# Optimization experiments

Measured on AMD Instinct MI355X. Metric: run time of the kernel, lower is better.

The kernel has to match this reference:

```python
import jax, jax.numpy as jnp
import numpy as np

NUM_USERS = 100000
NUM_ITEMS = 50000
DIM = 64
N_LAYERS = 3
L_W = 1e-4
E0 = 600000          # raw user-item interactions
B = 8192             # BPR batch size
N_NODES = NUM_USERS + NUM_ITEMS


def setup_inputs() -> dict:
    key = jax.random.key(0)
    k1, k2, k3, k4, k5, k6, k7 = jax.random.split(key, 7)
    return {
        "Gu": jax.random.normal(k1, (NUM_USERS, DIM), jnp.float32) * 0.1,
        "Gi": jax.random.normal(k2, (NUM_ITEMS, DIM), jnp.float32) * 0.1,
        "edge_user": jax.random.randint(k3, (E0,), 0, NUM_USERS),
        "edge_item": jax.random.randint(k4, (E0,), 0, NUM_ITEMS),
        "user": jax.random.randint(k5, (B,), 0, NUM_USERS),
        "pos": jax.random.randint(k6, (B,), 0, NUM_ITEMS),
        "neg": jax.random.randint(k7, (B,), 0, NUM_ITEMS),
    }


def _propagate(Gu, Gi, src, dst):
    # symmetric normalized adjacency (gcn_norm, no self-loops, as in LGConv)
    deg = jax.ops.segment_sum(jnp.ones_like(src, jnp.float32), dst,
                              num_segments=N_NODES)
    dinv = jnp.where(deg > 0, jax.lax.rsqrt(deg), 0.0)
    w = dinv[src] * dinv[dst]                      # [E]
    x = jnp.concatenate([Gu, Gi], axis=0)          # [N, D]
    acc = x
    h = x
    for _ in range(N_LAYERS):
        # SpMM: h' = D^-1/2 A D^-1/2 h  (gather + weighted scatter-add)
        h = jax.ops.segment_sum(w[:, None] * h[src], dst,
                                num_segments=N_NODES)
        acc = acc + h
    emb = acc / (N_LAYERS + 1)                     # mean over all layers
    return emb[:NUM_USERS], emb[NUM_USERS:]


def reference(Gu, Gi, edge_user, edge_item, user, pos, neg):
    # symmetrize bipartite edges; items offset by NUM_USERS
    src = jnp.concatenate([edge_user, edge_item + NUM_USERS])
    dst = jnp.concatenate([edge_item + NUM_USERS, edge_user])
    gu, gi = _propagate(Gu, Gi, src, dst)
    gu_u, gi_p, gi_n = gu[user], gi[pos], gi[neg]  # [B, D]
    xu_pos = jnp.sum(gu_u * gi_p, axis=1)
    xu_neg = jnp.sum(gu_u * gi_n, axis=1)
    mf_loss = -jnp.mean(jax.nn.log_sigmoid(xu_pos - xu_neg))
    reg = L_W * 0.5 * (jnp.sum(gu_u ** 2) + jnp.sum(gi_p ** 2)
                       + jnp.sum(gi_n ** 2)) / B
    return mf_loss + reg
```

## Files before the change

kernel.cpp:

```cpp
#include <hip/hip_runtime.h>

#define NUSERS 100000
#define NITEMS 50000
#define NNODES 150000
#define DIM 64
#define E0 600000
#define E2 (2 * E0)
#define BB 8192
#define LW 1e-4f
#define NN16 150016
#define LOSS_BLOCKS 128
#define UBLK 6250
#define IBLK 3125

#define NBUCK 1172
#define CHUNK_E 2048
#define CHUNKS 293
#define CPAD 320
#define BCAP 3072

__device__ __forceinline__ float bf_lo(unsigned u) { return __uint_as_float(u << 16); }
__device__ __forceinline__ float bf_hi(unsigned u) { return __uint_as_float(u & 0xffff0000u); }
__device__ __forceinline__ unsigned rne16(float x) {
  unsigned u = __float_as_uint(x);
  return (u + 0x7fffu + ((u >> 16) & 1u)) >> 16;
}
__device__ __forceinline__ unsigned pack2(float lo, float hi) {
  return rne16(lo) | (rne16(hi) << 16);
}

__global__ __launch_bounds__(256) void k_bcount(const int* __restrict__ eu,
                                                const int* __restrict__ ei,
                                                int* __restrict__ cnt) {
  __shared__ int h[NBUCK];
  for (int i = threadIdx.x; i < NBUCK; i += 256) h[i] = 0;
  __syncthreads();
  int c = blockIdx.x;
  int e0 = c * CHUNK_E;
  int e1 = min(e0 + CHUNK_E, E0);
  for (int e = e0 + threadIdx.x; e < e1; e += 256) {
    int u = eu[e];
    int it = NUSERS + ei[e];
    atomicAdd(&h[u >> 7], 1);
    atomicAdd(&h[it >> 7], 1);
  }
  __syncthreads();
  for (int i = threadIdx.x; i < NBUCK; i += 256) cnt[(size_t)i * CPAD + c] = h[i];
}

__global__ __launch_bounds__(256) void k_bscan1(int* __restrict__ cnt,
                                                int* __restrict__ btot) {
  int b = blockIdx.x * 4 + (threadIdx.x >> 6);
  int lane = threadIdx.x & 63;
  int* row = cnt + (size_t)b * CPAD;
  int carry = 0;
  for (int c0 = 0; c0 < CHUNKS; c0 += 64) {
    int c = c0 + lane;
    int v = (c < CHUNKS) ? row[c] : 0;
    int s = v;
    #pragma unroll
    for (int m = 1; m < 64; m <<= 1) {
      int t = __shfl_up(s, m);
      if (lane >= m) s += t;
    }
    if (c < CHUNKS) row[c] = carry + s - v;
    carry += __shfl(s, 63);
  }
  if (lane == 63) btot[b] = carry;
}

__global__ void k_bbase(const int* __restrict__ btot, int* __restrict__ bbase) {
  __shared__ int s[1024];
  int t = threadIdx.x;
  int i0 = 2 * t, i1 = 2 * t + 1;
  int v0 = (i0 < NBUCK) ? btot[i0] : 0;
  int v1 = (i1 < NBUCK) ? btot[i1] : 0;
  s[t] = v0 + v1;
  __syncthreads();
  for (int off = 1; off < 1024; off <<= 1) {
    int x = 0;
    if (t >= off) x = s[t - off];
    __syncthreads();
    if (t >= off) s[t] += x;
    __syncthreads();
  }
  int base = (t > 0) ? s[t - 1] : 0;
  if (i0 < NBUCK) bbase[i0] = base;
  if (i1 < NBUCK) bbase[i1] = base + v0;
}

__global__ __launch_bounds__(256) void k_bscatter(const int* __restrict__ eu,
                                                  const int* __restrict__ ei,
                                                  const int* __restrict__ cnt,
                                                  const int* __restrict__ bbase,
                                                  unsigned* __restrict__ pk) {
  __shared__ int soff[NBUCK];
  int c = blockIdx.x;
  for (int i = threadIdx.x; i < NBUCK; i += 256)
    soff[i] = cnt[(size_t)i * CPAD + c] + bbase[i];
  __syncthreads();
  int e0 = c * CHUNK_E;
  int e1 = min(e0 + CHUNK_E, E0);
  for (int e = e0 + threadIdx.x; e < e1; e += 256) {
    int u = eu[e];
    int it = NUSERS + ei[e];
    int s1 = atomicAdd(&soff[u >> 7], 1);
    pk[s1] = ((unsigned)it << 7) | (unsigned)(u & 127);
    int s2 = atomicAdd(&soff[it >> 7], 1);
    pk[s2] = ((unsigned)u << 7) | (unsigned)(it & 127);
  }
}

__global__ __launch_bounds__(256) void k_bucket_csr(
    const unsigned* __restrict__ pk, const int* __restrict__ btot,
    const int* __restrict__ bbase, int* __restrict__ deg, int* __restrict__ ptr,
    float* __restrict__ dinv, int* __restrict__ col,
    const float4* __restrict__ Gu4, const float4* __restrict__ Gi4,
    uint2* __restrict__ h0) {
  __shared__ unsigned sitm[BCAP];
  __shared__ int ldeg[128], lscan[128], lcnt[128];
  __shared__ float sdv[128];
  int b = blockIdx.x;
  int base = bbase[b];
  int n = btot[b];
  for (int i = threadIdx.x; i < n; i += 256)
    if (i < BCAP) sitm[i] = pk[base + i];
  if (threadIdx.x < 128) { ldeg[threadIdx.x] = 0; lcnt[threadIdx.x] = 0; }
  __syncthreads();
  for (int i = threadIdx.x; i < n; i += 256) {
    unsigned p = (i < BCAP) ? sitm[i] : pk[base + i];
    atomicAdd(&ldeg[p & 127], 1);
  }
  __syncthreads();
  if (threadIdx.x < 128) lscan[threadIdx.x] = ldeg[threadIdx.x];
  __syncthreads();
  for (int off = 1; off < 128; off <<= 1) {
    int t = 0;
    if (threadIdx.x < 128 && (int)threadIdx.x >= off) t = lscan[threadIdx.x - off];
    __syncthreads();
    if (threadIdx.x < 128 && (int)threadIdx.x >= off) lscan[threadIdx.x] += t;
    __syncthreads();
  }
  int node = b * 128 + threadIdx.x;
  if (threadIdx.x < 128) {
    int d = ldeg[threadIdx.x];
    lscan[threadIdx.x] -= d;
    float dv = d > 0 ? rsqrtf((float)d) : 0.0f;
    sdv[threadIdx.x] = dv;
    if (node < NNODES) {
      deg[node] = d;
      ptr[node] = base + lscan[threadIdx.x];
      dinv[node] = dv;
    }
  }
  __syncthreads();
  for (int i = threadIdx.x; i < n; i += 256) {
    unsigned p = (i < BCAP) ? sitm[i] : pk[base + i];
    int dl = p & 127;
    int pos = base + lscan[dl] + atomicAdd(&lcnt[dl], 1);
    col[pos] = (int)(p >> 7);
  }
  for (int w = threadIdx.x; w < 128 * 16; w += 256) {
    int nl = w >> 4, q = w & 15;
    int nd = b * 128 + nl;
    if (nd < NNODES) {
      float dv = sdv[nl];
      float4 v = (nd < NUSERS) ? Gu4[(size_t)nd * 16 + q]
                               : Gi4[(size_t)(nd - NUSERS) * 16 + q];
      h0[(size_t)nd * 16 + q] =
          make_uint2(pack2(dv * v.x, dv * v.y), pack2(dv * v.z, dv * v.w));
    }
  }
}

__global__ __launch_bounds__(512) void k_spmm2(
    const int* __restrict__ ptr, const int* __restrict__ deg,
    const int* __restrict__ col, const float* __restrict__ dinv,
    const uint4* __restrict__ h, uint4* __restrict__ hout) {
  int wid = threadIdx.x >> 6;
  int lane = threadIdx.x & 63;
  int sub = lane >> 3;
  int q = lane & 7;
  int gA, coff;
  const uint4* hsrc;
  if (blockIdx.x < UBLK) {
    gA = blockIdx.x * 16 + wid * 2;
    coff = NUSERS;
    hsrc = h + (size_t)NUSERS * 8;
  } else {
    gA = NUSERS + (blockIdx.x - UBLK) * 16 + wid * 2;
    coff = 0;
    hsrc = h;
  }
  int gB = gA + 1;
  int stA = ptr[gA], dgA = deg[gA];
  int stB = ptr[gB], dgB = deg[gB];
  float dnA = dinv[gA], dnB = dinv[gB];
  int cA = (sub < dgA) ? col[stA + sub] : -1;
  int cB = (sub < dgB) ? col[stB + sub] : -1;
  uint4 xA = {0, 0, 0, 0}, xB = {0, 0, 0, 0};
  if (cA >= 0) xA = hsrc[(size_t)(cA - coff) * 8 + q];
  if (cB >= 0) xB = hsrc[(size_t)(cB - coff) * 8 + q];
  float aA0 = bf_lo(xA.x), aA1 = bf_hi(xA.x), aA2 = bf_lo(xA.y), aA3 = bf_hi(xA.y);
  float aA4 = bf_lo(xA.z), aA5 = bf_hi(xA.z), aA6 = bf_lo(xA.w), aA7 = bf_hi(xA.w);
  float aB0 = bf_lo(xB.x), aB1 = bf_hi(xB.x), aB2 = bf_lo(xB.y), aB3 = bf_hi(xB.y);
  float aB4 = bf_lo(xB.z), aB5 = bf_hi(xB.z), aB6 = bf_lo(xB.w), aB7 = bf_hi(xB.w);
  for (int j = stA + 8 + sub; j < stA + dgA; j += 8) {
    int c = col[j];
    uint4 x = hsrc[(size_t)(c - coff) * 8 + q];
    aA0 += bf_lo(x.x); aA1 += bf_hi(x.x); aA2 += bf_lo(x.y); aA3 += bf_hi(x.y);
    aA4 += bf_lo(x.z); aA5 += bf_hi(x.z); aA6 += bf_lo(x.w); aA7 += bf_hi(x.w);
  }
  for (int j = stB + 8 + sub; j < stB + dgB; j += 8) {
    int c = col[j];
    uint4 x = hsrc[(size_t)(c - coff) * 8 + q];
    aB0 += bf_lo(x.x); aB1 += bf_hi(x.x); aB2 += bf_lo(x.y); aB3 += bf_hi(x.y);
    aB4 += bf_lo(x.z); aB5 += bf_hi(x.z); aB6 += bf_lo(x.w); aB7 += bf_hi(x.w);
  }
  #pragma unroll
  for (int m = 8; m <= 32; m <<= 1) {
    aA0 += __shfl_xor(aA0, m); aA1 += __shfl_xor(aA1, m);
    aA2 += __shfl_xor(aA2, m); aA3 += __shfl_xor(aA3, m);
    aA4 += __shfl_xor(aA4, m); aA5 += __shfl_xor(aA5, m);
    aA6 += __shfl_xor(aA6, m); aA7 += __shfl_xor(aA7, m);
    aB0 += __shfl_xor(aB0, m); aB1 += __shfl_xor(aB1, m);
    aB2 += __shfl_xor(aB2, m); aB3 += __shfl_xor(aB3, m);
    aB4 += __shfl_xor(aB4, m); aB5 += __shfl_xor(aB5, m);
    aB6 += __shfl_xor(aB6, m); aB7 += __shfl_xor(aB7, m);
  }
  if (sub == 0) {
    float sA = dnA * dnA;
    float sB = dnB * dnB;
    hout[(size_t)gA * 8 + q] = make_uint4(pack2(aA0 * sA, aA1 * sA), pack2(aA2 * sA, aA3 * sA),
                                          pack2(aA4 * sA, aA5 * sA), pack2(aA6 * sA, aA7 * sA));
    hout[(size_t)gB * 8 + q] = make_uint4(pack2(aB0 * sB, aB1 * sB), pack2(aB2 * sB, aB3 * sB),
                                          pack2(aB4 * sB, aB5 * sB), pack2(aB6 * sB, aB7 * sB));
  }
}

__device__ __forceinline__ int decode_node(int k, const int* __restrict__ usr,
                                           const int* __restrict__ pos,
                                           const int* __restrict__ neg, int* coff) {
  if (k < BB) { *coff = NUSERS; return usr[k]; }
  if (k < 2 * BB) { *coff = 0; return NUSERS + pos[k - BB]; }
  *coff = 0; return NUSERS + neg[k - 2 * BB];
}

__global__ __launch_bounds__(512) void k_spmm_batch(
    const int* __restrict__ usr, const int* __restrict__ pos, const int* __restrict__ neg,
    const int* __restrict__ ptr, const int* __restrict__ deg,
    const int* __restrict__ col, const float* __restrict__ dinv,
    const uint4* __restrict__ h, uint4* __restrict__ hout) {
  int wid = threadIdx.x >> 6;
  int lane = threadIdx.x & 63;
  int sub = lane >> 3;
  int q = lane & 7;
  int k0 = blockIdx.x * 16 + wid * 2;
  int cofA, cofB;
  int gA = decode_node(k0, usr, pos, neg, &cofA);
  int gB = decode_node(k0 + 1, usr, pos, neg, &cofB);
  const uint4* hsA = h + (size_t)cofA * 8;
  const uint4* hsB = h + (size_t)cofB * 8;
  int stA = ptr[gA], dgA = deg[gA];
  int stB = ptr[gB], dgB = deg[gB];
  float dnA = dinv[gA], dnB = dinv[gB];
  int cA = (sub < dgA) ? col[stA + sub] : -1;
  int cB = (sub < dgB) ? col[stB + sub] : -1;
  uint4 xA = {0, 0, 0, 0}, xB = {0, 0, 0, 0};
  if (cA >= 0) xA = hsA[(size_t)(cA - cofA) * 8 + q];
  if (cB >= 0) xB = hsB[(size_t)(cB - cofB) * 8 + q];
  float aA0 = bf_lo(xA.x), aA1 = bf_hi(xA.x), aA2 = bf_lo(xA.y), aA3 = bf_hi(xA.y);
  float aA4 = bf_lo(xA.z), aA5 = bf_hi(xA.z), aA6 = bf_lo(xA.w), aA7 = bf_hi(xA.w);
  float aB0 = bf_lo(xB.x), aB1 = bf_hi(xB.x), aB2 = bf_lo(xB.y), aB3 = bf_hi(xB.y);
  float aB4 = bf_lo(xB.z), aB5 = bf_hi(xB.z), aB6 = bf_lo(xB.w), aB7 = bf_hi(xB.w);
  for (int j = stA + 8 + sub; j < stA + dgA; j += 8) {
    int c = col[j];
    uint4 x = hsA[(size_t)(c - cofA) * 8 + q];
    aA0 += bf_lo(x.x); aA1 += bf_hi(x.x); aA2 += bf_lo(x.y); aA3 += bf_hi(x.y);
    aA4 += bf_lo(x.z); aA5 += bf_hi(x.z); aA6 += bf_lo(x.w); aA7 += bf_hi(x.w);
  }
  for (int j = stB + 8 + sub; j < stB + dgB; j += 8) {
    int c = col[j];
    uint4 x = hsB[(size_t)(c - cofB) * 8 + q];
    aB0 += bf_lo(x.x); aB1 += bf_hi(x.x); aB2 += bf_lo(x.y); aB3 += bf_hi(x.y);
    aB4 += bf_lo(x.z); aB5 += bf_hi(x.z); aB6 += bf_lo(x.w); aB7 += bf_hi(x.w);
  }
  #pragma unroll
  for (int m = 8; m <= 32; m <<= 1) {
    aA0 += __shfl_xor(aA0, m); aA1 += __shfl_xor(aA1, m);
    aA2 += __shfl_xor(aA2, m); aA3 += __shfl_xor(aA3, m);
    aA4 += __shfl_xor(aA4, m); aA5 += __shfl_xor(aA5, m);
    aA6 += __shfl_xor(aA6, m); aA7 += __shfl_xor(aA7, m);
    aB0 += __shfl_xor(aB0, m); aB1 += __shfl_xor(aB1, m);
    aB2 += __shfl_xor(aB2, m); aB3 += __shfl_xor(aB3, m);
    aB4 += __shfl_xor(aB4, m); aB5 += __shfl_xor(aB5, m);
    aB6 += __shfl_xor(aB6, m); aB7 += __shfl_xor(aB7, m);
  }
  if (sub == 0) {
    float sA = dnA * dnA;
    float sB = dnB * dnB;
    hout[(size_t)gA * 8 + q] = make_uint4(pack2(aA0 * sA, aA1 * sA), pack2(aA2 * sA, aA3 * sA),
                                          pack2(aA4 * sA, aA5 * sA), pack2(aA6 * sA, aA7 * sA));
    hout[(size_t)gB * 8 + q] = make_uint4(pack2(aB0 * sB, aB1 * sB), pack2(aB2 * sB, aB3 * sB),
                                          pack2(aB4 * sB, aB5 * sB), pack2(aB6 * sB, aB7 * sB));
  }
}

__global__ void k_loss(const int* __restrict__ usr, const int* __restrict__ pos,
                       const int* __restrict__ neg, const int* __restrict__ deg,
                       const float4* __restrict__ Gu4, const float4* __restrict__ Gi4,
                       const uint2* __restrict__ h1, const uint2* __restrict__ h2,
                       const uint2* __restrict__ h3, float* __restrict__ bpart) {
  __shared__ float sL[4], sR[4];
  int wid = threadIdx.x >> 6;
  int lane = threadIdx.x & 63;
  int r = lane >> 4;
  int q = lane & 15;
  int gw = blockIdx.x * 4 + wid;
  int nw = gridDim.x * 4;
  const float s = 0.25f;
  float accL = 0.0f, accR = 0.0f;
  for (int b4 = gw; b4 < BB / 4; b4 += nw) {
    int b = b4 * 4 + r;
    int iu = usr[b], ip = pos[b], ig = neg[b];
    float sdu = sqrtf((float)deg[iu]);
    float sdp = sqrtf((float)deg[NUSERS + ip]);
    float sdn = sqrtf((float)deg[NUSERS + ig]);
    size_t ou = (size_t)iu * 16 + q;
    size_t op = ((size_t)NUSERS + ip) * 16 + q;
    size_t on = ((size_t)NUSERS + ig) * 16 + q;
    float4 u = Gu4[ou];
    float4 p = Gi4[(size_t)ip * 16 + q];
    float4 g = Gi4[(size_t)ig * 16 + q];
    float4 su = {0, 0, 0, 0}, sp = {0, 0, 0, 0}, sg = {0, 0, 0, 0};
    uint2 v;
    v = h1[ou]; su.x += bf_lo(v.x); su.y += bf_hi(v.x); su.z += bf_lo(v.y); su.w += bf_hi(v.y);
    v = h2[ou]; su.x += bf_lo(v.x); su.y += bf_hi(v.x); su.z += bf_lo(v.y); su.w += bf_hi(v.y);
    v = h3[ou]; su.x += bf_lo(v.x); su.y += bf_hi(v.x); su.z += bf_lo(v.y); su.w += bf_hi(v.y);
    v = h1[op]; sp.x += bf_lo(v.x); sp.y += bf_hi(v.x); sp.z += bf_lo(v.y); sp.w += bf_hi(v.y);
    v = h2[op]; sp.x += bf_lo(v.x); sp.y += bf_hi(v.x); sp.z += bf_lo(v.y); sp.w += bf_hi(v.y);
    v = h3[op]; sp.x += bf_lo(v.x); sp.y += bf_hi(v.x); sp.z += bf_lo(v.y); sp.w += bf_hi(v.y);
    v = h1[on]; sg.x += bf_lo(v.x); sg.y += bf_hi(v.x); sg.z += bf_lo(v.y); sg.w += bf_hi(v.y);
    v = h2[on]; sg.x += bf_lo(v.x); sg.y += bf_hi(v.x); sg.z += bf_lo(v.y); sg.w += bf_hi(v.y);
    v = h3[on]; sg.x += bf_lo(v.x); sg.y += bf_hi(v.x); sg.z += bf_lo(v.y); sg.w += bf_hi(v.y);
    u.x = (u.x + sdu * su.x) * s; u.y = (u.y + sdu * su.y) * s;
    u.z = (u.z + sdu * su.z) * s; u.w = (u.w + sdu * su.w) * s;
    p.x = (p.x + sdp * sp.x) * s; p.y = (p.y + sdp * sp.y) * s;
    p.z = (p.z + sdp * sp.z) * s; p.w = (p.w + sdp * sp.w) * s;
    g.x = (g.x + sdn * sg.x) * s; g.y = (g.y + sdn * sg.y) * s;
    g.z = (g.z + sdn * sg.z) * s; g.w = (g.w + sdn * sg.w) * s;
    float dp = u.x * p.x + u.y * p.y + u.z * p.z + u.w * p.w;
    float dn = u.x * g.x + u.y * g.y + u.z * g.z + u.w * g.w;
    float rg = u.x * u.x + u.y * u.y + u.z * u.z + u.w * u.w
             + p.x * p.x + p.y * p.y + p.z * p.z + p.w * p.w
             + g.x * g.x + g.y * g.y + g.z * g.z + g.w * g.w;
    #pragma unroll
    for (int m = 1; m <= 8; m <<= 1) {
      dp += __shfl_xor(dp, m);
      dn += __shfl_xor(dn, m);
      rg += __shfl_xor(rg, m);
    }
    if (q == 0) {
      float diff = dp - dn;
      accL -= fminf(diff, 0.0f) - log1pf(expf(-fabsf(diff)));
      accR += rg;
    }
  }
  accL += __shfl_xor(accL, 16); accR += __shfl_xor(accR, 16);
  accL += __shfl_xor(accL, 32); accR += __shfl_xor(accR, 32);
  if (lane == 0) { sL[wid] = accL; sR[wid] = accR; }
  __syncthreads();
  if (threadIdx.x == 0) {
    bpart[blockIdx.x] = sL[0] + sL[1] + sL[2] + sL[3];
    bpart[LOSS_BLOCKS + blockIdx.x] = sR[0] + sR[1] + sR[2] + sR[3];
  }
}

__global__ void k_final(const float* __restrict__ bpart, float* __restrict__ out) {
  int lane = threadIdx.x;
  float l = bpart[lane] + bpart[lane + 64];
  float r = bpart[LOSS_BLOCKS + lane] + bpart[LOSS_BLOCKS + lane + 64];
  for (int off = 32; off > 0; off >>= 1) {
    l += __shfl_down(l, off);
    r += __shfl_down(r, off);
  }
  if (lane == 0) out[0] = l * (1.0f / BB) + LW * 0.5f * r * (1.0f / BB);
}

extern "C" void kernel_launch(void* const* d_in, const int* in_sizes, int n_in,
                              void* d_out, int out_size, void* d_ws, size_t ws_size,
                              hipStream_t stream) {
  const float* Gu = (const float*)d_in[0];
  const float* Gi = (const float*)d_in[1];
  const int* eu  = (const int*)d_in[2];
  const int* ei  = (const int*)d_in[3];
  const int* usr = (const int*)d_in[4];
  const int* pos = (const int*)d_in[5];
  const int* neg = (const int*)d_in[6];
  float* out = (float*)d_out;

  int* deg    = (int*)d_ws;
  int* ptr    = deg + NN16;
  float* dinv = (float*)(ptr + NN16);
  int* col    = (int*)(dinv + NN16);
  uint2* h0   = (uint2*)(col + E2);
  uint2* h1   = h0 + (size_t)NNODES * 16;
  uint2* h2   = h1 + (size_t)NNODES * 16;
  uint2* h3   = h2 + (size_t)NNODES * 16;
  float* bpart = (float*)(h3 + (size_t)NNODES * 16);

  unsigned* pk = (unsigned*)h1;
  int* cnt     = (int*)h2;
  int* btot    = (int*)h3;
  int* bbase   = btot + 1280;

  const float4* Gu4 = (const float4*)Gu;
  const float4* Gi4 = (const float4*)Gi;

  k_bcount<<<CHUNKS, 256, 0, stream>>>(eu, ei, cnt);
  k_bscan1<<<NBUCK / 4, 256, 0, stream>>>(cnt, btot);
  k_bbase<<<1, 1024, 0, stream>>>(btot, bbase);
  k_bscatter<<<CHUNKS, 256, 0, stream>>>(eu, ei, cnt, bbase, pk);
  k_bucket_csr<<<NBUCK, 256, 0, stream>>>(pk, btot, bbase, deg, ptr, dinv, col,
                                          Gu4, Gi4, h0);

  k_spmm2<<<UBLK + IBLK, 512, 0, stream>>>(ptr, deg, col, dinv,
                                           (const uint4*)h0, (uint4*)h1);
  k_spmm2<<<UBLK + IBLK, 512, 0, stream>>>(ptr, deg, col, dinv,
                                           (const uint4*)h1, (uint4*)h2);
  k_spmm_batch<<<(3 * BB) / 16, 512, 0, stream>>>(usr, pos, neg, ptr, deg, col, dinv,
                                                  (const uint4*)h2, (uint4*)h3);

  k_loss<<<LOSS_BLOCKS, 256, 0, stream>>>(usr, pos, neg, deg, Gu4, Gi4, h1, h2, h3, bpart);
  k_final<<<1, 64, 0, stream>>>(bpart, out);
}
```

Measured before the change: 242.7 us.

## Map one 8-lane group per node in SpMM instead of splitting edges across lanes

Both SpMM kernels stop giving each wave two nodes with edges split across eight sub-groups and a shuffle reduction. Each 8-thread group now owns one node and walks its whole neighbour list serially, two edges per iteration. This removes the shuffle reduction and the idle lanes on low-degree nodes, at the cost of per-lane load imbalance when degrees vary. The loss kernel also moves from 128 to 512 blocks, and the final reduction loops over the larger partial array.

```diff
diff --git a/kernel.cpp b/kernel.cpp
--- a/kernel.cpp
+++ b/kernel.cpp
@@ -9,9 +9,9 @@
 #define BB 8192
 #define LW 1e-4f
 #define NN16 150016
-#define LOSS_BLOCKS 128
-#define UBLK 6250
-#define IBLK 3125
+#define LOSS_BLOCKS 512
+#define SPMM_B 2344
+#define SPMMB_B 384
 
 #define NBUCK 1172
 #define CHUNK_E 2048
@@ -177,65 +177,38 @@
     const int* __restrict__ ptr, const int* __restrict__ deg,
     const int* __restrict__ col, const float* __restrict__ dinv,
     const uint4* __restrict__ h, uint4* __restrict__ hout) {
-  int wid = threadIdx.x >> 6;
-  int lane = threadIdx.x & 63;
-  int sub = lane >> 3;
-  int q = lane & 7;
-  int gA, coff;
+  int t = blockIdx.x * 512 + threadIdx.x;
+  int g = t >> 3;
+  int q = t & 7;
+  if (g >= NNODES) return;
+  int coff;
   const uint4* hsrc;
-  if (blockIdx.x < UBLK) {
-    gA = blockIdx.x * 16 + wid * 2;
-    coff = NUSERS;
-    hsrc = h + (size_t)NUSERS * 8;
-  } else {
-    gA = NUSERS + (blockIdx.x - UBLK) * 16 + wid * 2;
-    coff = 0;
-    hsrc = h;
-  }
-  int gB = gA + 1;
-  int stA = ptr[gA], dgA = deg[gA];
-  int stB = ptr[gB], dgB = deg[gB];
-  float dnA = dinv[gA], dnB = dinv[gB];
-  int cA = (sub < dgA) ? col[stA + sub] : -1;
-  int cB = (sub < dgB) ? col[stB + sub] : -1;
-  uint4 xA = {0, 0, 0, 0}, xB = {0, 0, 0, 0};
-  if (cA >= 0) xA = hsrc[(size_t)(cA - coff) * 8 + q];
-  if (cB >= 0) xB = hsrc[(size_t)(cB - coff) * 8 + q];
-  float aA0 = bf_lo(xA.x), aA1 = bf_hi(xA.x), aA2 = bf_lo(xA.y), aA3 = bf_hi(xA.y);
-  float aA4 = bf_lo(xA.z), aA5 = bf_hi(xA.z), aA6 = bf_lo(xA.w), aA7 = bf_hi(xA.w);
-  float aB0 = bf_lo(xB.x), aB1 = bf_hi(xB.x), aB2 = bf_lo(xB.y), aB3 = bf_hi(xB.y);
-  float aB4 = bf_lo(xB.z), aB5 = bf_hi(xB.z), aB6 = bf_lo(xB.w), aB7 = bf_hi(xB.w);
-  for (int j = stA + 8 + sub; j < stA + dgA; j += 8) {
-    int c = col[j];
-    uint4 x = hsrc[(size_t)(c - coff) * 8 + q];
-    aA0 += bf_lo(x.x); aA1 += bf_hi(x.x); aA2 += bf_lo(x.y); aA3 += bf_hi(x.y);
-    aA4 += bf_lo(x.z); aA5 += bf_hi(x.z); aA6 += bf_lo(x.w); aA7 += bf_hi(x.w);
-  }
-  for (int j = stB + 8 + sub; j < stB + dgB; j += 8) {
-    int c = col[j];
-    uint4 x = hsrc[(size_t)(c - coff) * 8 + q];
-    aB0 += bf_lo(x.x); aB1 += bf_hi(x.x); aB2 += bf_lo(x.y); aB3 += bf_hi(x.y);
-    aB4 += bf_lo(x.z); aB5 += bf_hi(x.z); aB6 += bf_lo(x.w); aB7 += bf_hi(x.w);
-  }
-  #pragma unroll
-  for (int m = 8; m <= 32; m <<= 1) {
-    aA0 += __shfl_xor(aA0, m); aA1 += __shfl_xor(aA1, m);
-    aA2 += __shfl_xor(aA2, m); aA3 += __shfl_xor(aA3, m);
-    aA4 += __shfl_xor(aA4, m); aA5 += __shfl_xor(aA5, m);
-    aA6 += __shfl_xor(aA6, m); aA7 += __shfl_xor(aA7, m);
-    aB0 += __shfl_xor(aB0, m); aB1 += __shfl_xor(aB1, m);
-    aB2 += __shfl_xor(aB2, m); aB3 += __shfl_xor(aB3, m);
-    aB4 += __shfl_xor(aB4, m); aB5 += __shfl_xor(aB5, m);
-    aB6 += __shfl_xor(aB6, m); aB7 += __shfl_xor(aB7, m);
-  }
-  if (sub == 0) {
-    float sA = dnA * dnA;
-    float sB = dnB * dnB;
-    hout[(size_t)gA * 8 + q] = make_uint4(pack2(aA0 * sA, aA1 * sA), pack2(aA2 * sA, aA3 * sA),
-                                          pack2(aA4 * sA, aA5 * sA), pack2(aA6 * sA, aA7 * sA));
-    hout[(size_t)gB * 8 + q] = make_uint4(pack2(aB0 * sB, aB1 * sB), pack2(aB2 * sB, aB3 * sB),
-                                          pack2(aB4 * sB, aB5 * sB), pack2(aB6 * sB, aB7 * sB));
-  }
+  if (g < NUSERS) { coff = NUSERS; hsrc = h + (size_t)NUSERS * 8; }
+  else { coff = 0; hsrc = h; }
+  int st = ptr[g], dg = deg[g];
+  float dn = dinv[g];
+  float a0 = 0, a1 = 0, a2 = 0, a3 = 0, a4 = 0, a5 = 0, a6 = 0, a7 = 0;
+  int jend = st + dg;
+  int j = st;
+  for (; j + 2 <= jend; j += 2) {
+    int c0 = col[j] - coff;
+    int c1 = col[j + 1] - coff;
+    uint4 x0 = hsrc[(size_t)c0 * 8 + q];
+    uint4 x1 = hsrc[(size_t)c1 * 8 + q];
+    a0 += bf_lo(x0.x); a1 += bf_hi(x0.x); a2 += bf_lo(x0.y); a3 += bf_hi(x0.y);
+    a4 += bf_lo(x0.z); a5 += bf_hi(x0.z); a6 += bf_lo(x0.w); a7 += bf_hi(x0.w);
+    a0 += bf_lo(x1.x); a1 += bf_hi(x1.x); a2 += bf_lo(x1.y); a3 += bf_hi(x1.y);
+    a4 += bf_lo(x1.z); a5 += bf_hi(x1.z); a6 += bf_lo(x1.w); a7 += bf_hi(x1.w);
+  }
+  if (j < jend) {
+    int c0 = col[j] - coff;
+    uint4 x0 = hsrc[(size_t)c0 * 8 + q];
+    a0 += bf_lo(x0.x); a1 += bf_hi(x0.x); a2 += bf_lo(x0.y); a3 += bf_hi(x0.y);
+    a4 += bf_lo(x0.z); a5 += bf_hi(x0.z); a6 += bf_lo(x0.w); a7 += bf_hi(x0.w);
+  }
+  float s = dn * dn;
+  hout[(size_t)g * 8 + q] = make_uint4(pack2(a0 * s, a1 * s), pack2(a2 * s, a3 * s),
+                                       pack2(a4 * s, a5 * s), pack2(a6 * s, a7 * s));
 }
 
 __device__ __forceinline__ int decode_node(int k, const int* __restrict__ usr,
@@ -251,59 +224,36 @@
     const int* __restrict__ ptr, const int* __restrict__ deg,
     const int* __restrict__ col, const float* __restrict__ dinv,
     const uint4* __restrict__ h, uint4* __restrict__ hout) {
-  int wid = threadIdx.x >> 6;
-  int lane = threadIdx.x & 63;
-  int sub = lane >> 3;
-  int q = lane & 7;
-  int k0 = blockIdx.x * 16 + wid * 2;
-  int cofA, cofB;
-  int gA = decode_node(k0, usr, pos, neg, &cofA);
-  int gB = decode_node(k0 + 1, usr, pos, neg, &cofB);
-  const uint4* hsA = h + (size_t)cofA * 8;
-  const uint4* hsB = h + (size_t)cofB * 8;
-  int stA = ptr[gA], dgA = deg[gA];
-  int stB = ptr[gB], dgB = deg[gB];
-  float dnA = dinv[gA], dnB = dinv[gB];
-  int cA = (sub < dgA) ? col[stA + sub] : -1;
-  int cB = (sub < dgB) ? col[stB + sub] : -1;
-  uint4 xA = {0, 0, 0, 0}, xB = {0, 0, 0, 0};
-  if (cA >= 0) xA = hsA[(size_t)(cA - cofA) * 8 + q];
-  if (cB >= 0) xB = hsB[(size_t)(cB - cofB) * 8 + q];
-  float aA0 = bf_lo(xA.x), aA1 = bf_hi(xA.x), aA2 = bf_lo(xA.y), aA3 = bf_hi(xA.y);
-  float aA4 = bf_lo(xA.z), aA5 = bf_hi(xA.z), aA6 = bf_lo(xA.w), aA7 = bf_hi(xA.w);
-  float aB0 = bf_lo(xB.x), aB1 = bf_hi(xB.x), aB2 = bf_lo(xB.y), aB3 = bf_hi(xB.y);
-  float aB4 = bf_lo(xB.z), aB5 = bf_hi(xB.z), aB6 = bf_lo(xB.w), aB7 = bf_hi(xB.w);
-  for (int j = stA + 8 + sub; j < stA + dgA; j += 8) {
-    int c = col[j];
-    uint4 x = hsA[(size_t)(c - cofA) * 8 + q];
-    aA0 += bf_lo(x.x); aA1 += bf_hi(x.x); aA2 += bf_lo(x.y); aA3 += bf_hi(x.y);
-    aA4 += bf_lo(x.z); aA5 += bf_hi(x.z); aA6 += bf_lo(x.w); aA7 += bf_hi(x.w);
-  }
-  for (int j = stB + 8 + sub; j < stB + dgB; j += 8) {
-    int c = col[j];
-    uint4 x = hsB[(size_t)(c - cofB) * 8 + q];
-    aB0 += bf_lo(x.x); aB1 += bf_hi(x.x); aB2 += bf_lo(x.y); aB3 += bf_hi(x.y);
-    aB4 += bf_lo(x.z); aB5 += bf_hi(x.z); aB6 += bf_lo(x.w); aB7 += bf_hi(x.w);
-  }
-  #pragma unroll
-  for (int m = 8; m <= 32; m <<= 1) {
-    aA0 += __shfl_xor(aA0, m); aA1 += __shfl_xor(aA1, m);
-    aA2 += __shfl_xor(aA2, m); aA3 += __shfl_xor(aA3, m);
-    aA4 += __shfl_xor(aA4, m); aA5 += __shfl_xor(aA5, m);
-    aA6 += __shfl_xor(aA6, m); aA7 += __shfl_xor(aA7, m);
-    aB0 += __shfl_xor(aB0, m); aB1 += __shfl_xor(aB1, m);
-    aB2 += __shfl_xor(aB2, m); aB3 += __shfl_xor(aB3, m);
-    aB4 += __shfl_xor(aB4, m); aB5 += __shfl_xor(aB5, m);
-    aB6 += __shfl_xor(aB6, m); aB7 += __shfl_xor(aB7, m);
-  }
-  if (sub == 0) {
-    float sA = dnA * dnA;
-    float sB = dnB * dnB;
-    hout[(size_t)gA * 8 + q] = make_uint4(pack2(aA0 * sA, aA1 * sA), pack2(aA2 * sA, aA3 * sA),
-                                          pack2(aA4 * sA, aA5 * sA), pack2(aA6 * sA, aA7 * sA));
-    hout[(size_t)gB * 8 + q] = make_uint4(pack2(aB0 * sB, aB1 * sB), pack2(aB2 * sB, aB3 * sB),
-                                          pack2(aB4 * sB, aB5 * sB), pack2(aB6 * sB, aB7 * sB));
-  }
+  int t = blockIdx.x * 512 + threadIdx.x;
+  int k = t >> 3;
+  int q = t & 7;
+  int coff;
+  int g = decode_node(k, usr, pos, neg, &coff);
+  const uint4* hsrc = h + (size_t)coff * 8;
+  int st = ptr[g], dg = deg[g];
+  float dn = dinv[g];
+  float a0 = 0, a1 = 0, a2 = 0, a3 = 0, a4 = 0, a5 = 0, a6 = 0, a7 = 0;
+  int jend = st + dg;
+  int j = st;
+  for (; j + 2 <= jend; j += 2) {
+    int c0 = col[j] - coff;
+    int c1 = col[j + 1] - coff;
+    uint4 x0 = hsrc[(size_t)c0 * 8 + q];
+    uint4 x1 = hsrc[(size_t)c1 * 8 + q];
+    a0 += bf_lo(x0.x); a1 += bf_hi(x0.x); a2 += bf_lo(x0.y); a3 += bf_hi(x0.y);
+    a4 += bf_lo(x0.z); a5 += bf_hi(x0.z); a6 += bf_lo(x0.w); a7 += bf_hi(x0.w);
+    a0 += bf_lo(x1.x); a1 += bf_hi(x1.x); a2 += bf_lo(x1.y); a3 += bf_hi(x1.y);
+    a4 += bf_lo(x1.z); a5 += bf_hi(x1.z); a6 += bf_lo(x1.w); a7 += bf_hi(x1.w);
+  }
+  if (j < jend) {
+    int c0 = col[j] - coff;
+    uint4 x0 = hsrc[(size_t)c0 * 8 + q];
+    a0 += bf_lo(x0.x); a1 += bf_hi(x0.x); a2 += bf_lo(x0.y); a3 += bf_hi(x0.y);
+    a4 += bf_lo(x0.z); a5 += bf_hi(x0.z); a6 += bf_lo(x0.w); a7 += bf_hi(x0.w);
+  }
+  float s = dn * dn;
+  hout[(size_t)g * 8 + q] = make_uint4(pack2(a0 * s, a1 * s), pack2(a2 * s, a3 * s),
+                                       pack2(a4 * s, a5 * s), pack2(a6 * s, a7 * s));
 }
 
 __global__ void k_loss(const int* __restrict__ usr, const int* __restrict__ pos,
@@ -378,8 +328,12 @@
 
 __global__ void k_final(const float* __restrict__ bpart, float* __restrict__ out) {
   int lane = threadIdx.x;
-  float l = bpart[lane] + bpart[lane + 64];
-  float r = bpart[LOSS_BLOCKS + lane] + bpart[LOSS_BLOCKS + lane + 64];
+  float l = 0.0f, r = 0.0f;
+  #pragma unroll
+  for (int i = 0; i < LOSS_BLOCKS; i += 64) {
+    l += bpart[lane + i];
+    r += bpart[LOSS_BLOCKS + lane + i];
+  }
   for (int off = 32; off > 0; off >>= 1) {
     l += __shfl_down(l, off);
     r += __shfl_down(r, off);
@@ -424,12 +378,12 @@
   k_bucket_csr<<<NBUCK, 256, 0, stream>>>(pk, btot, bbase, deg, ptr, dinv, col,
                                           Gu4, Gi4, h0);
 
-  k_spmm2<<<UBLK + IBLK, 512, 0, stream>>>(ptr, deg, col, dinv,
-                                           (const uint4*)h0, (uint4*)h1);
-  k_spmm2<<<UBLK + IBLK, 512, 0, stream>>>(ptr, deg, col, dinv,
-                                           (const uint4*)h1, (uint4*)h2);
-  k_spmm_batch<<<(3 * BB) / 16, 512, 0, stream>>>(usr, pos, neg, ptr, deg, col, dinv,
-                                                  (const uint4*)h2, (uint4*)h3);
+  k_spmm2<<<SPMM_B, 512, 0, stream>>>(ptr, deg, col, dinv,
+                                      (const uint4*)h0, (uint4*)h1);
+  k_spmm2<<<SPMM_B, 512, 0, stream>>>(ptr, deg, col, dinv,
+                                      (const uint4*)h1, (uint4*)h2);
+  k_spmm_batch<<<SPMMB_B, 512, 0, stream>>>(usr, pos, neg, ptr, deg, col, dinv,
+                                            (const uint4*)h2, (uint4*)h3);
 
   k_loss<<<LOSS_BLOCKS, 256, 0, stream>>>(usr, pos, neg, deg, Gu4, Gi4, h1, h2, h3, bpart);
   k_final<<<1, 64, 0, stream>>>(bpart, out);
```

New measurement: 208.8 us. -14.0%, faster.
